# Optimization experiments

Measured on AMD Instinct MI355X. Metric: run time of the kernel, lower is better.

The kernel has to match this reference:

```python
import jax, jax.numpy as jnp
import numpy as np

N_HEAD = 16
LN_EPS = 1e-5


def _layernorm(x, g, b):
    m = x.mean(-1, keepdims=True)
    var = x.var(-1, keepdims=True)
    return (x - m) / jnp.sqrt(var + LN_EPS) * g + b


def setup_inputs() -> dict:
    key = jax.random.key(0)
    B, C, D = 4, 1024, 1024
    ks = jax.random.split(key, 8)
    std = 0.02  # trunc-normal-ish init scale
    inp = {
        "q": jax.random.normal(ks[0], (B, C, D), jnp.float32),
        "k": jax.random.normal(ks[1], (B, C, D), jnp.float32),
        "v": jax.random.normal(ks[2], (B, C, D), jnp.float32),
        # LayerNorm params for norm_k / norm_v (norm_q output is discarded in the source)
        "ln_k_g": jnp.ones((D,), jnp.float32), "ln_k_b": jnp.zeros((D,), jnp.float32),
        "ln_v_g": jnp.ones((D,), jnp.float32), "ln_v_b": jnp.zeros((D,), jnp.float32),
        # Linear projections (stored as [in, out]; x @ W + b)
        "Wq": jax.random.normal(ks[3], (D, D), jnp.float32) * std, "bq": jnp.zeros((D,), jnp.float32),
        "Wk": jax.random.normal(ks[4], (D, D), jnp.float32) * std, "bk": jnp.zeros((D,), jnp.float32),
        "Wv": jax.random.normal(ks[5], (D, D), jnp.float32) * std, "bv": jnp.zeros((D,), jnp.float32),
        "Wo": jax.random.normal(ks[6], (D, D), jnp.float32) * std, "bo": jnp.zeros((D,), jnp.float32),
    }
    return inp


def reference(q, k, v, ln_k_g, ln_k_b, ln_v_g, ln_v_b,
              Wq, bq, Wk, bk, Wv, bv, Wo, bo):
    B, C, D = q.shape
    H = N_HEAD
    Dh = D // H
    scale = Dh ** -0.5

    # Source quirk: q is projected WITHOUT layernorm (norm_q output discarded);
    # k and v are layernormed before projection.
    qp = q @ Wq + bq
    kp = _layernorm(k, ln_k_g, ln_k_b) @ Wk + bk
    vp = _layernorm(v, ln_v_g, ln_v_b) @ Wv + bv

    def split_heads(x):  # [B,C,D] -> [B,H,C,Dh]
        return x.reshape(B, C, H, Dh).transpose(0, 2, 1, 3)

    qh, kh, vh = split_heads(qp), split_heads(kp), split_heads(vp)

    # GELU-activated scores, then scale, then softmax (nonstandard ordering)
    scores = jnp.einsum('bhcd,bhkd->bhck', qh, kh)
    attn = jax.nn.softmax(jax.nn.gelu(scores, approximate=False) * scale, axis=-1)

    out = jnp.einsum('bhck,bhkd->bhcd', attn, vh)  # [B,H,C,Dh]
    out = out.transpose(0, 2, 1, 3).reshape(B, C, D)
    out = out @ Wo + bo
    # F.normalize(dim=-1): L2 normalize with eps clamp
    out = out / jnp.maximum(jnp.linalg.norm(out, axis=-1, keepdims=True), 1e-12)
    # dropout is identity in eval mode
    return out, attn
```

## Files before the change

kernel.cpp:

```cpp
#include <hip/hip_runtime.h>

typedef unsigned short u16;
typedef __attribute__((ext_vector_type(8))) short bf16x8;
typedef __attribute__((ext_vector_type(4))) float f32x4;

__device__ inline float b2f(u16 u) {
  unsigned x = ((unsigned)u) << 16;
  return __uint_as_float(x);
}
__device__ inline u16 f2b(float f) {
  unsigned u = __float_as_uint(f);
  unsigned r = (u + 0x7fffu + ((u >> 16) & 1u)) >> 16;
  return (u16)r;
}

__device__ inline float wsum(float x) {
#pragma unroll
  for (int o = 32; o > 0; o >>= 1) x += __shfl_down(x, o);
  return x;
}

__device__ inline void gl16(const u16* g, u16* l) {
  __builtin_amdgcn_global_load_lds((const __attribute__((address_space(1))) void*)g,
                                   (__attribute__((address_space(3))) void*)l, 16, 0, 0);
}

__global__ __launch_bounds__(256) void prep_kernel(const float* __restrict__ q,
                                                   const float* __restrict__ k,
                                                   const float* __restrict__ v,
                                                   const float* __restrict__ kg,
                                                   const float* __restrict__ kb,
                                                   const float* __restrict__ vg,
                                                   const float* __restrict__ vb,
                                                   u16* __restrict__ QB,
                                                   u16* __restrict__ LNK,
                                                   u16* __restrict__ LNV) {
  __shared__ float red[8];
  int blk = blockIdx.x;
  int mode = blk >> 12;
  long base = (long)(blk & 4095) * 1024;
  int t = threadIdx.x;
  const float* x = mode == 0 ? q : (mode == 1 ? k : v);
  u16* y = mode == 0 ? QB : (mode == 1 ? LNK : LNV);
  float4 raw = *(const float4*)(x + base + t * 4);
  float vv[4] = {raw.x, raw.y, raw.z, raw.w};
  if (mode == 0) {
    u16 o[4];
#pragma unroll
    for (int i = 0; i < 4; i++) o[i] = f2b(vv[i]);
    *(uint2*)(y + base + t * 4) = *(uint2*)o;
    return;
  }
  const float* g = mode == 1 ? kg : vg;
  const float* bb = mode == 1 ? kb : vb;
  float s = 0.f, ss = 0.f;
#pragma unroll
  for (int i = 0; i < 4; i++) { s += vv[i]; ss += vv[i] * vv[i]; }
  s = wsum(s);
  ss = wsum(ss);
  int wid = t >> 6;
  if ((t & 63) == 0) { red[wid] = s; red[4 + wid] = ss; }
  __syncthreads();
  s = red[0] + red[1] + red[2] + red[3];
  ss = red[4] + red[5] + red[6] + red[7];
  float mean = s * (1.f / 1024.f);
  float var = ss * (1.f / 1024.f) - mean * mean;
  float inv = rsqrtf(var + 1e-5f);
  float4 gv = *(const float4*)(g + t * 4);
  float4 bv = *(const float4*)(bb + t * 4);
  float gg[4] = {gv.x, gv.y, gv.z, gv.w};
  float b2[4] = {bv.x, bv.y, bv.z, bv.w};
  u16 outr[4];
#pragma unroll
  for (int i = 0; i < 4; i++) outr[i] = f2b((vv[i] - mean) * inv * gg[i] + b2[i]);
  *(uint2*)(y + base + t * 4) = *(uint2*)outr;
}

__global__ __launch_bounds__(256) void transpose_w4(const float* __restrict__ W0,
                                                    const float* __restrict__ W1,
                                                    const float* __restrict__ W2,
                                                    const float* __restrict__ W3,
                                                    u16* __restrict__ T0, u16* __restrict__ T1,
                                                    u16* __restrict__ T2, u16* __restrict__ T3) {
  int z = blockIdx.z;
  const float* src = z == 0 ? W0 : (z == 1 ? W1 : (z == 2 ? W2 : W3));
  u16* dst = z == 0 ? T0 : (z == 1 ? T1 : (z == 2 ? T2 : T3));
  __shared__ u16 tile[32][33];
  int tx = threadIdx.x & 31, ty = threadIdx.x >> 5;
  int x = blockIdx.x * 32 + tx;
  int y0 = blockIdx.y * 32;
#pragma unroll
  for (int i = 0; i < 32; i += 8) tile[ty + i][tx] = f2b(src[(long)(y0 + ty + i) * 1024 + x]);
  __syncthreads();
  int X = blockIdx.y * 32 + tx;
  int Y0 = blockIdx.x * 32;
#pragma unroll
  for (int i = 0; i < 32; i += 8) dst[(long)(Y0 + ty + i) * 1024 + X] = tile[tx][ty + i];
}

template <int BM, int BN, typename TC, bool TRANSV>
__device__ __forceinline__ void gemm_core(const u16* __restrict__ Ab,
                                          const u16* __restrict__ Bb,
                                          const float* __restrict__ bias,
                                          TC* __restrict__ Cb, long m0, long n0) {
  constexpr int TM = BM / 32;
  constexpr int TN = BN / 32;
  __shared__ __align__(16) u16 lsA[BM * 32];
  __shared__ __align__(16) u16 lsB[BN * 32];

  int tid = threadIdx.x;
  int wid = tid >> 6;
  int lane = tid & 63;
  int wm = (wid >> 1) * (BM / 2);
  int wn = (wid & 1) * (BN / 2);
  int lm = lane & 15;
  int quad = lane >> 4;

  f32x4 acc[TM][TN];
#pragma unroll
  for (int i = 0; i < TM; i++)
#pragma unroll
    for (int j = 0; j < TN; j++) acc[i][j] = (f32x4){0.f, 0.f, 0.f, 0.f};

  for (int k0 = 0; k0 < 1024; k0 += 32) {
#pragma unroll
    for (int c = tid; c < BM * 4; c += 256)
      gl16(Ab + (m0 + (c >> 2)) * 1024 + k0 + (c & 3) * 8, &lsA[c * 8]);
#pragma unroll
    for (int c = tid; c < BN * 4; c += 256)
      gl16(Bb + (n0 + (c >> 2)) * 1024 + k0 + (c & 3) * 8, &lsB[c * 8]);
    __syncthreads();
    bf16x8 af[TM], bfr[TN];
#pragma unroll
    for (int i = 0; i < TM; i++)
      af[i] = *(const bf16x8*)&lsA[(wm + i * 16 + lm) * 32 + quad * 8];
#pragma unroll
    for (int j = 0; j < TN; j++)
      bfr[j] = *(const bf16x8*)&lsB[(wn + j * 16 + lm) * 32 + quad * 8];
#pragma unroll
    for (int i = 0; i < TM; i++)
#pragma unroll
      for (int j = 0; j < TN; j++)
        acc[i][j] = __builtin_amdgcn_mfma_f32_16x16x32_bf16(af[i], bfr[j], acc[i][j], 0, 0, 0);
    __syncthreads();
  }

  if constexpr (TRANSV) {
#pragma unroll
    for (int j = 0; j < TN; j++) {
      long n = n0 + wn + j * 16 + lm;
      float bv = bias[n];
      int h = (int)(n >> 6), dh = (int)(n & 63);
#pragma unroll
      for (int i = 0; i < TM; i++) {
        long mb = m0 + wm + i * 16 + quad * 4;
        int bidx = (int)(mb >> 10);
        long c = mb & 1023;
        u16 pk[4];
#pragma unroll
        for (int r = 0; r < 4; r++) pk[r] = f2b(acc[i][j][r] + bv);
        *(uint2*)((u16*)Cb + ((long)(bidx * 16 + h) * 64 + dh) * 1024 + c) = *(uint2*)pk;
      }
    }
  } else {
#pragma unroll
    for (int j = 0; j < TN; j++) {
      long n = n0 + wn + j * 16 + lm;
      float bv = bias ? bias[n] : 0.f;
#pragma unroll
      for (int i = 0; i < TM; i++) {
        long mb = m0 + wm + i * 16 + quad * 4;
#pragma unroll
        for (int r = 0; r < 4; r++) {
          float val = acc[i][j][r] + bv;
          if constexpr (sizeof(TC) == 2) Cb[(mb + r) * 1024 + n] = f2b(val);
          else Cb[(mb + r) * 1024 + n] = val;
        }
      }
    }
  }
}

struct QKVArgs {
  const u16* A[3];
  const u16* B[3];
  const float* b[3];
  u16* C[3];
};

__global__ __launch_bounds__(256) void gemm_qkv(QKVArgs g) {
  int z = blockIdx.z;
  long m0 = (long)blockIdx.x * 128, n0 = (long)blockIdx.y * 128;
  if (z == 2)
    gemm_core<128, 128, u16, true>(g.A[2], g.B[2], g.b[2], g.C[2], m0, n0);
  else
    gemm_core<128, 128, u16, false>(g.A[z], g.B[z], g.b[z], g.C[z], m0, n0);
}

__global__ __launch_bounds__(256) void gemm_o(const u16* __restrict__ A,
                                              const u16* __restrict__ Bt,
                                              const float* __restrict__ bias,
                                              float* __restrict__ C) {
  gemm_core<128, 128, float, false>(A, Bt, bias, C, (long)blockIdx.x * 128,
                                    (long)blockIdx.y * 128);
}

__global__ __launch_bounds__(256) void fused_attn(const u16* __restrict__ QP,
                                                  const u16* __restrict__ KP,
                                                  const u16* __restrict__ VT,
                                                  float* __restrict__ attn,
                                                  u16* __restrict__ CTX) {
  __shared__ __align__(16) u16 P[16 * 1032];
  __shared__ __align__(16) u16 qt[16 * 72];
  __shared__ float wreds[4][16];

  int z = blockIdx.y;
  int b = z >> 4, h = z & 15;
  long q0 = (long)blockIdx.x * 16;
  int tid = threadIdx.x;
  int wid = tid >> 6, lane = tid & 63;
  int lm = lane & 15, quad = lane >> 4;

  const u16* Qb = QP + (long)b * 1048576 + (long)h * 64;
  const u16* Kb = KP + (long)b * 1048576 + (long)h * 64;
  const u16* Vz = VT + (long)z * 65536;
  float* Az = attn + (long)z * 1048576;

  if (tid < 128) {
    int row = tid >> 3, col8 = (tid & 7) * 8;
    *(uint4*)&qt[row * 72 + col8] = *(const uint4*)(Qb + (q0 + row) * 1024 + col8);
  }
  __syncthreads();

  bf16x8 qf0 = *(const bf16x8*)&qt[lm * 72 + quad * 8];
  bf16x8 qf1 = *(const bf16x8*)&qt[lm * 72 + 32 + quad * 8];

  int ncol0 = wid * 256;
  float sum = 0.f;
#pragma unroll
  for (int jj = 0; jj < 16; jj++) {
    const u16* kr = Kb + (long)(ncol0 + jj * 16 + lm) * 1024;
    bf16x8 kf0 = *(const bf16x8*)(kr + quad * 8);
    bf16x8 kf1 = *(const bf16x8*)(kr + 32 + quad * 8);
    f32x4 s = (f32x4){0.f, 0.f, 0.f, 0.f};
    __builtin_amdgcn_s_setprio(1);
    s = __builtin_amdgcn_mfma_f32_16x16x32_bf16(kf0, qf0, s, 0, 0, 0);
    s = __builtin_amdgcn_mfma_f32_16x16x32_bf16(kf1, qf1, s, 0, 0, 0);
    __builtin_amdgcn_s_setprio(0);
    u16 pk[4];
#pragma unroll
    for (int r = 0; r < 4; r++) {
      float x = s[r];
      float u = 0.70710678118654752f * x;
      float a = fabsf(u);
      float t = __builtin_amdgcn_rcpf(fmaf(0.3275911f, a, 1.0f));
      float p = t * fmaf(t, fmaf(t, fmaf(t, fmaf(t, 1.061405429f, -1.453152027f),
                                         1.421413741f), -0.284496736f), 0.254829592f);
      float eq = __expf(-a * a);
      float erfa = fmaf(-p, eq, 1.0f);
      float erfu = copysignf(erfa, u);
      float hx = 0.0625f * x;
      float logit = fmaf(hx, erfu, hx);
      float e = __expf(logit);
      sum += e;
      pk[r] = f2b(e);
    }
    *(uint2*)&P[lm * 1032 + ncol0 + jj * 16 + quad * 4] = *(uint2*)pk;
  }

  sum += __shfl_xor(sum, 16);
  sum += __shfl_xor(sum, 32);
  if (lane < 16) wreds[wid][lane] = sum;
  __syncthreads();

#pragma unroll
  for (int r = 0; r < 16; r++) {
    float inv = __builtin_amdgcn_rcpf(wreds[0][r] + wreds[1][r] + wreds[2][r] + wreds[3][r]);
    uint2 raw = *(const uint2*)&P[r * 1032 + tid * 4];
    u16* pr = (u16*)&raw;
    f32x4 o;
    o[0] = b2f(pr[0]) * inv;
    o[1] = b2f(pr[1]) * inv;
    o[2] = b2f(pr[2]) * inv;
    o[3] = b2f(pr[3]) * inv;
    __builtin_nontemporal_store(o, (f32x4*)(Az + (q0 + r) * 1024 + tid * 4));
  }

  {
    f32x4 a0 = (f32x4){0.f, 0.f, 0.f, 0.f};
    f32x4 a1 = a0, a2 = a0, a3 = a0;
    const u16* Vrow = Vz + (long)(wid * 16 + lm) * 1024;
#pragma unroll 2
    for (int kc = 0; kc < 1024; kc += 128) {
      bf16x8 p0 = *(const bf16x8*)&P[lm * 1032 + kc + quad * 8];
      bf16x8 v0 = *(const bf16x8*)(Vrow + kc + quad * 8);
      bf16x8 p1 = *(const bf16x8*)&P[lm * 1032 + kc + 32 + quad * 8];
      bf16x8 v1 = *(const bf16x8*)(Vrow + kc + 32 + quad * 8);
      bf16x8 p2 = *(const bf16x8*)&P[lm * 1032 + kc + 64 + quad * 8];
      bf16x8 v2 = *(const bf16x8*)(Vrow + kc + 64 + quad * 8);
      bf16x8 p3 = *(const bf16x8*)&P[lm * 1032 + kc + 96 + quad * 8];
      bf16x8 v3 = *(const bf16x8*)(Vrow + kc + 96 + quad * 8);
      __builtin_amdgcn_s_setprio(1);
      a0 = __builtin_amdgcn_mfma_f32_16x16x32_bf16(p0, v0, a0, 0, 0, 0);
      a1 = __builtin_amdgcn_mfma_f32_16x16x32_bf16(p1, v1, a1, 0, 0, 0);
      a2 = __builtin_amdgcn_mfma_f32_16x16x32_bf16(p2, v2, a2, 0, 0, 0);
      a3 = __builtin_amdgcn_mfma_f32_16x16x32_bf16(p3, v3, a3, 0, 0, 0);
      __builtin_amdgcn_s_setprio(0);
    }
    f32x4 acc = (a0 + a1) + (a2 + a3);
    int n = wid * 16 + lm;
    u16* Cb = CTX + (long)b * 1048576 + (long)h * 64;
#pragma unroll
    for (int r = 0; r < 4; r++) {
      int row = quad * 4 + r;
      float inv = __builtin_amdgcn_rcpf(wreds[0][row] + wreds[1][row] +
                                        wreds[2][row] + wreds[3][row]);
      Cb[(q0 + row) * 1024 + n] = f2b(acc[r] * inv);
    }
  }
}

__global__ __launch_bounds__(256) void l2norm_kernel(const float* __restrict__ o,
                                                     float* __restrict__ out) {
  long base = (long)blockIdx.x * 1024;
  int t = threadIdx.x;
  float4 raw = *(const float4*)(o + base + t * 4);
  float v[4] = {raw.x, raw.y, raw.z, raw.w};
  float ss = 0.f;
#pragma unroll
  for (int i = 0; i < 4; i++) ss += v[i] * v[i];
  ss = wsum(ss);
  __shared__ float red[4];
  int wid = t >> 6;
  if ((t & 63) == 0) red[wid] = ss;
  __syncthreads();
  ss = red[0] + red[1] + red[2] + red[3];
  float inv = 1.f / fmaxf(sqrtf(ss), 1e-12f);
  float4 outr = {v[0] * inv, v[1] * inv, v[2] * inv, v[3] * inv};
  *(float4*)(out + base + t * 4) = outr;
}

extern "C" void kernel_launch(void* const* d_in, const int* in_sizes, int n_in,
                              void* d_out, int out_size, void* d_ws, size_t ws_size,
                              hipStream_t stream) {
  const float* q = (const float*)d_in[0];
  const float* k = (const float*)d_in[1];
  const float* v = (const float*)d_in[2];
  const float* ln_k_g = (const float*)d_in[3];
  const float* ln_k_b = (const float*)d_in[4];
  const float* ln_v_g = (const float*)d_in[5];
  const float* ln_v_b = (const float*)d_in[6];
  const float* Wq = (const float*)d_in[7];
  const float* bq = (const float*)d_in[8];
  const float* Wk = (const float*)d_in[9];
  const float* bk = (const float*)d_in[10];
  const float* Wv = (const float*)d_in[11];
  const float* bv_ = (const float*)d_in[12];
  const float* Wo = (const float*)d_in[13];
  const float* bo = (const float*)d_in[14];

  const long MEG = 1024 * 1024;
  u16* ws16 = (u16*)d_ws;
  u16* LNK = ws16;
  u16* LNV = ws16 + 4 * MEG;
  u16* WQT = ws16 + 8 * MEG;
  u16* WKT = ws16 + 9 * MEG;
  u16* WVT = ws16 + 10 * MEG;
  u16* WOT = ws16 + 11 * MEG;
  u16* QP  = ws16 + 12 * MEG;
  u16* KP  = ws16 + 16 * MEG;
  u16* VT  = ws16 + 24 * MEG;
  u16* QB  = ws16 + 28 * MEG;
  u16* CTX = LNK;
  float* OO = (float*)(ws16 + 12 * MEG);

  float* out = (float*)d_out;
  float* attn = out + 4 * MEG;

  prep_kernel<<<12288, 256, 0, stream>>>(q, k, v, ln_k_g, ln_k_b, ln_v_g, ln_v_b, QB, LNK, LNV);

  transpose_w4<<<dim3(32, 32, 4), 256, 0, stream>>>(Wq, Wk, Wv, Wo, WQT, WKT, WVT, WOT);

  QKVArgs ga;
  ga.A[0] = QB;  ga.A[1] = LNK; ga.A[2] = LNV;
  ga.B[0] = WQT; ga.B[1] = WKT; ga.B[2] = WVT;
  ga.b[0] = bq;  ga.b[1] = bk;  ga.b[2] = bv_;
  ga.C[0] = QP;  ga.C[1] = KP;  ga.C[2] = VT;
  gemm_qkv<<<dim3(32, 8, 3), 256, 0, stream>>>(ga);

  fused_attn<<<dim3(64, 64), 256, 0, stream>>>(QP, KP, VT, attn, CTX);

  gemm_o<<<dim3(32, 8), 256, 0, stream>>>(CTX, WOT, bo, OO);

  l2norm_kernel<<<4096, 256, 0, stream>>>(OO, out);
}
```

Measured before the change: 503.3 us.

## Double GEMM K-tile to 64 with XOR-swizzled LDS and direct Q loads

The shared GEMM core now stages 64-wide K tiles instead of 32, which halves the number of barrier pairs per output tile. The LDS layout uses an XOR swizzle on the 16-byte chunk index to avoid bank conflicts on the MFMA fragment reads. Launch bounds on both GEMM kernels now request 4 blocks per CU. The attention kernel also drops its shared Q staging and barrier, loading Q fragments straight from global memory. The cost is double the LDS per block, which may limit occupancy.

```diff
diff --git a/kernel.cpp b/kernel.cpp
--- a/kernel.cpp
+++ b/kernel.cpp
@@ -105,8 +105,8 @@
                                           TC* __restrict__ Cb, long m0, long n0) {
   constexpr int TM = BM / 32;
   constexpr int TN = BN / 32;
-  __shared__ __align__(16) u16 lsA[BM * 32];
-  __shared__ __align__(16) u16 lsB[BN * 32];
+  __shared__ __align__(16) u16 lsA[BM * 64];
+  __shared__ __align__(16) u16 lsB[BN * 64];
 
   int tid = threadIdx.x;
   int wid = tid >> 6;
@@ -122,26 +122,38 @@
 #pragma unroll
     for (int j = 0; j < TN; j++) acc[i][j] = (f32x4){0.f, 0.f, 0.f, 0.f};
 
-  for (int k0 = 0; k0 < 1024; k0 += 32) {
-#pragma unroll
-    for (int c = tid; c < BM * 4; c += 256)
-      gl16(Ab + (m0 + (c >> 2)) * 1024 + k0 + (c & 3) * 8, &lsA[c * 8]);
-#pragma unroll
-    for (int c = tid; c < BN * 4; c += 256)
-      gl16(Bb + (n0 + (c >> 2)) * 1024 + k0 + (c & 3) * 8, &lsB[c * 8]);
+  for (int k0 = 0; k0 < 1024; k0 += 64) {
+#pragma unroll
+    for (int c = tid; c < BM * 8; c += 256) {
+      int row = c >> 3, g = c & 7;
+      gl16(Ab + (m0 + row) * 1024 + k0 + ((g ^ (row & 7)) * 8), &lsA[c * 8]);
+    }
+#pragma unroll
+    for (int c = tid; c < BN * 8; c += 256) {
+      int row = c >> 3, g = c & 7;
+      gl16(Bb + (n0 + row) * 1024 + k0 + ((g ^ (row & 7)) * 8), &lsB[c * 8]);
+    }
     __syncthreads();
-    bf16x8 af[TM], bfr[TN];
-#pragma unroll
-    for (int i = 0; i < TM; i++)
-      af[i] = *(const bf16x8*)&lsA[(wm + i * 16 + lm) * 32 + quad * 8];
-#pragma unroll
-    for (int j = 0; j < TN; j++)
-      bfr[j] = *(const bf16x8*)&lsB[(wn + j * 16 + lm) * 32 + quad * 8];
-#pragma unroll
-    for (int i = 0; i < TM; i++)
-#pragma unroll
-      for (int j = 0; j < TN; j++)
-        acc[i][j] = __builtin_amdgcn_mfma_f32_16x16x32_bf16(af[i], bfr[j], acc[i][j], 0, 0, 0);
+#pragma unroll
+    for (int kk = 0; kk < 2; kk++) {
+      bf16x8 af[TM], bfr[TN];
+      int gi = kk * 4 + quad;
+#pragma unroll
+      for (int i = 0; i < TM; i++) {
+        int row = wm + i * 16 + lm;
+        af[i] = *(const bf16x8*)&lsA[row * 64 + ((gi ^ (row & 7)) * 8)];
+      }
+#pragma unroll
+      for (int j = 0; j < TN; j++) {
+        int row = wn + j * 16 + lm;
+        bfr[j] = *(const bf16x8*)&lsB[row * 64 + ((gi ^ (row & 7)) * 8)];
+      }
+#pragma unroll
+      for (int i = 0; i < TM; i++)
+#pragma unroll
+        for (int j = 0; j < TN; j++)
+          acc[i][j] = __builtin_amdgcn_mfma_f32_16x16x32_bf16(af[i], bfr[j], acc[i][j], 0, 0, 0);
+    }
     __syncthreads();
   }
 
@@ -188,7 +200,7 @@
   u16* C[3];
 };
 
-__global__ __launch_bounds__(256) void gemm_qkv(QKVArgs g) {
+__global__ __launch_bounds__(256, 4) void gemm_qkv(QKVArgs g) {
   int z = blockIdx.z;
   long m0 = (long)blockIdx.x * 128, n0 = (long)blockIdx.y * 128;
   if (z == 2)
@@ -197,10 +209,10 @@
     gemm_core<128, 128, u16, false>(g.A[z], g.B[z], g.b[z], g.C[z], m0, n0);
 }
 
-__global__ __launch_bounds__(256) void gemm_o(const u16* __restrict__ A,
-                                              const u16* __restrict__ Bt,
-                                              const float* __restrict__ bias,
-                                              float* __restrict__ C) {
+__global__ __launch_bounds__(256, 4) void gemm_o(const u16* __restrict__ A,
+                                                 const u16* __restrict__ Bt,
+                                                 const float* __restrict__ bias,
+                                                 float* __restrict__ C) {
   gemm_core<128, 128, float, false>(A, Bt, bias, C, (long)blockIdx.x * 128,
                                     (long)blockIdx.y * 128);
 }
@@ -211,7 +223,6 @@
                                                   float* __restrict__ attn,
                                                   u16* __restrict__ CTX) {
   __shared__ __align__(16) u16 P[16 * 1032];
-  __shared__ __align__(16) u16 qt[16 * 72];
   __shared__ float wreds[4][16];
 
   int z = blockIdx.y;
@@ -226,14 +237,9 @@
   const u16* Vz = VT + (long)z * 65536;
   float* Az = attn + (long)z * 1048576;
 
-  if (tid < 128) {
-    int row = tid >> 3, col8 = (tid & 7) * 8;
-    *(uint4*)&qt[row * 72 + col8] = *(const uint4*)(Qb + (q0 + row) * 1024 + col8);
-  }
-  __syncthreads();
-
-  bf16x8 qf0 = *(const bf16x8*)&qt[lm * 72 + quad * 8];
-  bf16x8 qf1 = *(const bf16x8*)&qt[lm * 72 + 32 + quad * 8];
+  const u16* qr = Qb + (q0 + lm) * 1024;
+  bf16x8 qf0 = *(const bf16x8*)(qr + quad * 8);
+  bf16x8 qf1 = *(const bf16x8*)(qr + 32 + quad * 8);
 
   int ncol0 = wid * 256;
   float sum = 0.f;
```

After: 504.7 us. Within noise of the previous version (+0.3%).
